# Optimization experiments

Hardware: AMD Instinct MI355X
Metric: run time of the kernel (lower is better)

Reference implementation:

```python
import jax, jax.numpy as jnp
import numpy as np

N, B, FD, D, MSG, SCN, H, FFN = 2048, 16, 128, 32, 32, 16, 4, 64
HD = D // H


def _lin(k, o, i, scale=0.05):
    kw, kb = jax.random.split(k)
    return (jax.random.normal(kw, (o, i), jnp.float32) * scale,
            jax.random.normal(kb, (o,), jnp.float32) * scale)


def setup_inputs() -> dict:
    key = jax.random.key(0)
    ks = jax.random.split(key, 24)
    inp = {}
    inp['src'] = jax.random.randint(ks[0], (B,), 0, N)
    inp['dst'] = jax.random.randint(ks[1], (B,), 0, N)
    inp['edge_feat'] = jax.random.normal(ks[2], (B, 3), jnp.float32)
    inp['timestamps'] = jax.random.uniform(ks[3], (B,), dtype=jnp.float32)
    inp['node_features'] = jax.random.normal(ks[4], (N, FD), jnp.float32)
    inp['adj'] = jnp.zeros((N, N), jnp.float32)  # unused: assume_identity_adj=True
    inp['memory'] = jax.random.normal(ks[5], (N, D), jnp.float32) * 0.1
    inp['W_emb'], inp['b_emb'] = _lin(ks[6], D, FD)
    inp['Wqkv'], inp['bqkv'] = _lin(ks[7], 3 * D, D)
    inp['Wo'], inp['bo'] = _lin(ks[8], D, D)
    inp['g1'] = jnp.ones((D,), jnp.float32); inp['be1'] = jnp.zeros((D,), jnp.float32)
    inp['g2'] = jnp.ones((D,), jnp.float32); inp['be2'] = jnp.zeros((D,), jnp.float32)
    inp['W_f1'], inp['b_f1'] = _lin(ks[9], FFN, D)
    inp['W_f2'], inp['b_f2'] = _lin(ks[10], D, FFN)
    inp['W_scn'], inp['b_scn'] = _lin(ks[11], SCN, D)
    inp['g_scn'] = jnp.ones((SCN,), jnp.float32); inp['be_scn'] = jnp.zeros((SCN,), jnp.float32)
    inp['W_e1'], inp['b_e1'] = _lin(ks[12], 32, 2 * SCN)
    inp['W_e2'], inp['b_e2'] = _lin(ks[13], 16, 32)
    inp['W_e3'], inp['b_e3'] = _lin(ks[14], 1, 16)
    inp['gru_Wih'], inp['gru_bih'] = _lin(ks[15], 3 * D, MSG)
    inp['gru_Whh'], inp['gru_bhh'] = _lin(ks[16], 3 * D, D)
    inp['W_m1'], inp['b_m1'] = _lin(ks[17], MSG, 2 * D + 3)
    inp['W_m2'], inp['b_m2'] = _lin(ks[18], MSG, MSG)
    return inp


def _ln(x, g, b):
    mu = x.mean(-1, keepdims=True)
    var = ((x - mu) ** 2).mean(-1, keepdims=True)
    return (x - mu) * jax.lax.rsqrt(var + 1e-5) * g + b


def _gru(x, h, Wih, Whh, bih, bhh):
    # torch.nn.GRUCell semantics
    gi = x @ Wih.T + bih
    gh = h @ Whh.T + bhh
    ir, iz, i_n = jnp.split(gi, 3, -1)
    hr, hz, h_n = jnp.split(gh, 3, -1)
    r = jax.nn.sigmoid(ir + hr)
    z = jax.nn.sigmoid(iz + hz)
    n = jnp.tanh(i_n + r * h_n)
    return (1.0 - z) * n + z * h


def _update_memory(memory, src, dst, edge_feat,
                   gru_Wih, gru_Whh, gru_bih, gru_bhh, W_m1, b_m1, W_m2, b_m2):
    # messages computed from pre-update memory (as in torch source)
    msg_in = jnp.concatenate([memory[src], memory[dst], edge_feat], axis=1)  # [B, 2D+3]
    messages = jax.nn.relu(msg_in @ W_m1.T + b_m1) @ W_m2.T + b_m2           # [B, MSG]

    def step(mem, inp):
        s, d, m = inp
        hs = _gru(m, mem[s], gru_Wih, gru_Whh, gru_bih, gru_bhh)
        mem = mem.at[s].set(hs)
        hd = _gru(m, mem[d], gru_Wih, gru_Whh, gru_bih, gru_bhh)  # sees updated mem if d==s earlier
        mem = mem.at[d].set(hd)
        return mem, None

    new_mem, _ = jax.lax.scan(step, memory, (src, dst, messages))
    return new_mem


def _edge_logits(node_features, src, dst,
                 W_emb, b_emb, Wqkv, bqkv, Wo, bo, g1, be1, g2, be2,
                 W_f1, b_f1, W_f2, b_f2, W_scn, b_scn, g_scn, be_scn,
                 W_e1, b_e1, W_e2, b_e2, W_e3, b_e3):
    x0 = node_features @ W_emb.T + b_emb                      # [N, D]
    x = jnp.broadcast_to(x0[None], (B, N, D))                 # [B, N, D]
    # --- Graph transformer layer (MHA, eval mode: dropout = identity) ---
    qkv = x @ Wqkv.T + bqkv                                   # [B, N, 3D]
    q, k, v = jnp.split(qkv, 3, -1)
    q = q.reshape(B, N, H, HD)
    k = k.reshape(B, N, H, HD)
    v = v.reshape(B, N, H, HD)
    scores = jnp.einsum('bqhd,bkhd->bhqk', q, k) / np.sqrt(HD)
    attn = jax.nn.softmax(scores, axis=-1)
    ao = jnp.einsum('bhqk,bkhd->bqhd', attn, v).reshape(B, N, D)
    ao = ao @ Wo.T + bo
    x = _ln(x + ao, g1, be1)
    ffn = jax.nn.gelu(x @ W_f1.T + b_f1, approximate=False) @ W_f2.T + b_f2
    x = _ln(x + ffn, g2, be2)
    # --- SCN layer (identity adjacency assumed) ---
    s_out = jax.nn.relu(_ln(x @ W_scn.T + b_scn, g_scn, be_scn))  # [B, N, SCN]
    bi = jnp.arange(B)
    src_emb = s_out[bi, src]
    dst_emb = s_out[bi, dst]
    h = jnp.concatenate([src_emb, dst_emb], axis=-1)
    h = jax.nn.relu(h @ W_e1.T + b_e1)
    h = jax.nn.relu(h @ W_e2.T + b_e2)
    return (h @ W_e3.T + b_e3).squeeze(-1)                    # [B]


def reference(src, dst, edge_feat, timestamps, node_features, adj, memory,
              W_emb, b_emb, Wqkv, bqkv, Wo, bo, g1, be1, g2, be2,
              W_f1, b_f1, W_f2, b_f2, W_scn, b_scn, g_scn, be_scn,
              W_e1, b_e1, W_e2, b_e2, W_e3, b_e3,
              gru_Wih, gru_bih, gru_Whh, gru_bhh, W_m1, b_m1, W_m2, b_m2):
    new_mem = _update_memory(memory, src, dst, edge_feat,
                             gru_Wih, gru_Whh, gru_bih, gru_bhh,
                             W_m1, b_m1, W_m2, b_m2)
    edge_logit = _edge_logits(node_features, src, dst,
                              W_emb, b_emb, Wqkv, bqkv, Wo, bo, g1, be1, g2, be2,
                              W_f1, b_f1, W_f2, b_f2, W_scn, b_scn, g_scn, be_scn,
                              W_e1, b_e1, W_e2, b_e2, W_e3, b_e3)
    return edge_logit, new_mem
```

## Files before the change

### kernel.cpp

```cpp
#include <hip/hip_runtime.h>
#include <math.h>

#define NN   2048
#define BB   16

#define WS_X0   0
#define WS_QT   65536
#define WS_KT   131072
#define WS_VT   196608
#define WS_PART 262144
#define WS_GI   268800

__device__ __forceinline__ float sigmoidf_(float x) { return 1.0f / (1.0f + __expf(-x)); }
__device__ __forceinline__ float tanhf_(float x) {
    float ex = __expf(2.0f * x);
    return 1.0f - 2.0f / (ex + 1.0f);
}
__device__ __forceinline__ float dot4_(float4 a, float4 b) {
    return a.x*b.x + a.y*b.y + a.z*b.z + a.w*b.w;
}

__global__ __launch_bounds__(256) void k1_embed_qkv_msg(
    const float* __restrict__ nf, const float* __restrict__ Wemb, const float* __restrict__ bemb,
    const float* __restrict__ Wqkv, const float* __restrict__ bqkv,
    const float* __restrict__ mem, const int* __restrict__ src, const int* __restrict__ dst,
    const float* __restrict__ ef,
    const float* __restrict__ Wm1, const float* __restrict__ bm1,
    const float* __restrict__ Wm2, const float* __restrict__ bm2,
    const float* __restrict__ Wih, const float* __restrict__ bih,
    float* __restrict__ ws, float* __restrict__ out)
{
    __shared__ float We_s[32 * 130];
    __shared__ float nf_s[8 * 130];
    __shared__ float x0_s[8 * 33];
    __shared__ float Wq_s[96 * 33];
    __shared__ __align__(16) float Wm1_s[2144];
    __shared__ float Wm2_s[32 * 33];
    __shared__ float Wih_s[96 * 33];
    __shared__ float min_s[67];
    __shared__ float mr_s[32];
    __shared__ float msg_s[32];

    const int t = threadIdx.x, bx = blockIdx.x;
    const bool domsg = (bx < 16);

    float4 rA[4], rB[3], rC;
    #pragma unroll
    for (int k = 0; k < 4; ++k) rA[k] = ((const float4*)Wemb)[t + 256 * k];
    #pragma unroll
    for (int k = 0; k < 3; ++k) rB[k] = ((const float4*)Wqkv)[t + 256 * k];
    rC = ((const float4*)nf)[bx * 256 + t];

    float4 rm1[3], rm2v, rih[3];
    float rminv = 0.f;
    if (domsg) {
        #pragma unroll
        for (int k = 0; k < 3; ++k) {
            int idx = t + 256 * k;
            rm1[k] = (idx < 536) ? ((const float4*)Wm1)[idx] : make_float4(0,0,0,0);
        }
        rm2v = ((const float4*)Wm2)[t];
        #pragma unroll
        for (int k = 0; k < 3; ++k) rih[k] = ((const float4*)Wih)[t + 256 * k];
        if (t < 67) {
            const int e = bx;
            rminv = (t < 32) ? mem[src[e] * 32 + t]
                  : (t < 64) ? mem[dst[e] * 32 + (t - 32)]
                             : ef[e * 3 + (t - 64)];
        }
    }

    if (bx >= 16 && bx < 80) {
        int g = (bx - 16) * 256 + t;
        ((float4*)(out + 16))[g] = ((const float4*)mem)[g];
    }

    #pragma unroll
    for (int k = 0; k < 4; ++k) {
        int idx = t + 256 * k;
        int r = idx >> 5, c = (idx & 31) * 4;
        We_s[r * 130 + c] = rA[k].x; We_s[r * 130 + c + 1] = rA[k].y;
        We_s[r * 130 + c + 2] = rA[k].z; We_s[r * 130 + c + 3] = rA[k].w;
    }
    #pragma unroll
    for (int k = 0; k < 3; ++k) {
        int idx = t + 256 * k;
        int r = idx >> 3, c = (idx & 7) * 4;
        Wq_s[r * 33 + c] = rB[k].x; Wq_s[r * 33 + c + 1] = rB[k].y;
        Wq_s[r * 33 + c + 2] = rB[k].z; Wq_s[r * 33 + c + 3] = rB[k].w;
    }
    {
        int r = t >> 5, c = (t & 31) * 4;
        nf_s[r * 130 + c] = rC.x; nf_s[r * 130 + c + 1] = rC.y;
        nf_s[r * 130 + c + 2] = rC.z; nf_s[r * 130 + c + 3] = rC.w;
    }
    if (domsg) {
        #pragma unroll
        for (int k = 0; k < 3; ++k) {
            int idx = t + 256 * k;
            if (idx < 536) ((float4*)Wm1_s)[idx] = rm1[k];
        }
        { int r = t >> 3, c = (t & 7) * 4;
          Wm2_s[r * 33 + c] = rm2v.x; Wm2_s[r * 33 + c + 1] = rm2v.y;
          Wm2_s[r * 33 + c + 2] = rm2v.z; Wm2_s[r * 33 + c + 3] = rm2v.w; }
        #pragma unroll
        for (int k = 0; k < 3; ++k) {
            int idx = t + 256 * k;
            int r = idx >> 3, c = (idx & 7) * 4;
            Wih_s[r * 33 + c] = rih[k].x; Wih_s[r * 33 + c + 1] = rih[k].y;
            Wih_s[r * 33 + c + 2] = rih[k].z; Wih_s[r * 33 + c + 3] = rih[k].w;
        }
        if (t < 67) min_s[t] = rminv;
    }
    __syncthreads();

    const int j = t >> 5, o = t & 31;
    const int n = bx * 8 + j;

    float acc = bemb[o];
    {
        const float2* Wr = (const float2*)&We_s[o * 130];
        const float2* Nr = (const float2*)&nf_s[j * 130];
        float sx = 0.f, sy = 0.f;
        #pragma unroll 16
        for (int i = 0; i < 64; ++i) {
            float2 w = Wr[i], x = Nr[i];
            sx += w.x * x.x; sy += w.y * x.y;
        }
        acc += sx + sy;
    }
    x0_s[j * 33 + o] = acc;
    ws[WS_X0 + n * 32 + o] = acc;
    if (domsg && t < 32) {
        float a1 = bm1[t];
        for (int i = 0; i < 67; ++i) a1 += Wm1_s[t * 67 + i] * min_s[i];
        mr_s[t] = fmaxf(a1, 0.f);
    }
    __syncthreads();

    #pragma unroll
    for (int c = 0; c < 3; ++c) {
        int oo = c * 32 + o;
        float a2 = bqkv[oo];
        #pragma unroll 8
        for (int i = 0; i < 32; ++i) a2 += Wq_s[oo * 33 + i] * x0_s[j * 33 + i];
        int h = o >> 3, d = o & 7;
        float* base = ws + (c == 0 ? WS_QT : (c == 1 ? WS_KT : WS_VT));
        base[h * 16384 + n * 8 + d] = a2;
    }
    if (domsg && t < 32) {
        float a2 = bm2[t];
        #pragma unroll 8
        for (int i = 0; i < 32; ++i) a2 += Wm2_s[t * 33 + i] * mr_s[i];
        msg_s[t] = a2;
    }
    __syncthreads();

    if (domsg && t < 96) {
        float a3 = bih[t];
        #pragma unroll 8
        for (int i = 0; i < 32; ++i) a3 += Wih_s[t * 33 + i] * msg_s[i];
        ws[WS_GI + bx * 96 + t] = a3;
    }
}

__global__ __launch_bounds__(256) void k2_attn(
    const int* __restrict__ src, const int* __restrict__ dst,
    float* __restrict__ ws)
{
    const int t = threadIdx.x, bx = blockIdx.x;
    const int s  = bx >> 2;
    const int ks = bx & 3;
    const int h  = t >> 6;
    const int l  = t & 63;

    const int e = s >> 1;
    const int n = (s & 1) ? dst[e] : src[e];

    const float* qg = ws + WS_QT + h * 16384 + n * 8;
    const float4 qa  = *(const float4*)qg;
    const float4 qb4 = *(const float4*)(qg + 4);
    const float* kbase = ws + WS_KT + h * 16384;
    const float* vbase = ws + WS_VT + h * 16384;

    float4 oa = make_float4(0.f, 0.f, 0.f, 0.f);
    float4 ob = make_float4(0.f, 0.f, 0.f, 0.f);
    float ssum = 0.f;
    const float scale = 0.35355339059327373f;

    #pragma unroll
    for (int i = 0; i < 8; ++i) {
        const int key = ks * 512 + i * 64 + l;
        const float4 ka = *(const float4*)(kbase + key * 8);
        const float4 kb = *(const float4*)(kbase + key * 8 + 4);
        const float sc = (dot4_(qa, ka) + dot4_(qb4, kb)) * scale;
        const float p = __expf(sc);
        ssum += p;
        const float4 va = *(const float4*)(vbase + key * 8);
        const float4 vb = *(const float4*)(vbase + key * 8 + 4);
        oa.x += p * va.x; oa.y += p * va.y; oa.z += p * va.z; oa.w += p * va.w;
        ob.x += p * vb.x; ob.y += p * vb.y; ob.z += p * vb.z; ob.w += p * vb.w;
    }

    #pragma unroll
    for (int m = 1; m <= 32; m <<= 1) {
        ssum += __shfl_xor(ssum, m);
        oa.x += __shfl_xor(oa.x, m); oa.y += __shfl_xor(oa.y, m);
        oa.z += __shfl_xor(oa.z, m); oa.w += __shfl_xor(oa.w, m);
        ob.x += __shfl_xor(ob.x, m); ob.y += __shfl_xor(ob.y, m);
        ob.z += __shfl_xor(ob.z, m); ob.w += __shfl_xor(ob.w, m);
    }
    if (l == 0) {
        float* p = ws + WS_PART + ((s * 4 + h) * 4 + ks) * 12;
        *(float4*)p       = oa;
        *(float4*)(p + 4) = ob;
        p[8] = ssum;
    }
}

__global__ __launch_bounds__(256, 1) void k34_post_scan(
    const int* __restrict__ src, const int* __restrict__ dst,
    const float* __restrict__ mem,
    const float* __restrict__ Wo, const float* __restrict__ bo,
    const float* __restrict__ g1, const float* __restrict__ be1,
    const float* __restrict__ Wf1, const float* __restrict__ bf1,
    const float* __restrict__ Wf2, const float* __restrict__ bf2,
    const float* __restrict__ g2, const float* __restrict__ be2,
    const float* __restrict__ Wscn, const float* __restrict__ bscn,
    const float* __restrict__ gscn, const float* __restrict__ bescn,
    const float* __restrict__ Whh, const float* __restrict__ bhh,
    const float* __restrict__ We1, const float* __restrict__ be1e,
    const float* __restrict__ We2, const float* __restrict__ be2e,
    const float* __restrict__ We3, const float* __restrict__ be3,
    float* __restrict__ ws, float* __restrict__ out)
{
    __shared__ float arow[32 * 33];
    __shared__ float x1s[32 * 33];
    __shared__ float fs[32 * 65];
    __shared__ __align__(16) float slots[32 * 36];
    __shared__ int nid_s[32], prev_s[32], round_s[32], last_s[32];
    __shared__ int list_s[32], cnt_s, maxr_s;

    const int t = threadIdx.x;
    const int j0 = t >> 5, o = t & 31;
    const int l = t & 63, w = t >> 6;
    const bool lowhalf = (l < 32);

    float4 w1[8], w2[8], w3[8];
    const int r2 = lowhalf ? l + 64 : l - 32;
    const int r3 = l + 32;
    #pragma unroll
    for (int c = 0; c < 8; ++c) {
        w1[c] = ((const float4*)Whh)[l * 8 + c];
        w2[c] = ((const float4*)Whh)[r2 * 8 + c];
        w3[c] = ((const float4*)Whh)[r3 * 8 + c];
    }
    const float b1 = bhh[l], b2 = bhh[r2], b3 = bhh[r3];

    if (t < 32) nid_s[t] = (t & 1) ? dst[t >> 1] : src[t >> 1];

    #pragma unroll 1
    for (int si = 0; si < 4; ++si) {
        const int jj = si * 8 + j0;
        const int ej = jj >> 1;
        const int n = (jj & 1) ? dst[ej] : src[ej];
        const int h = o >> 3, d = o & 7;
        float num = 0.f, den = 0.f;
        #pragma unroll
        for (int ks = 0; ks < 4; ++ks) {
            const float* p = ws + WS_PART + ((jj * 4 + h) * 4 + ks) * 12;
            num += p[d];
            den += p[8];
        }
        arow[jj * 33 + o] = num / den;
        fs[jj * 65 + o] = ws[WS_X0 + n * 32 + o];
    }
    __syncthreads();

    if (t < 32) {
        const int me = nid_s[t];
        int pv = -1, rd = 0;
        for (int j2 = 0; j2 < t; ++j2) if (nid_s[j2] == me) { pv = j2; ++rd; }
        prev_s[t] = pv; round_s[t] = rd;
        int isl = 1;
        for (int j2 = t + 1; j2 < 32; ++j2) if (nid_s[j2] == me) { isl = 0; break; }
        last_s[t] = isl;
        int mr = rd;
        #pragma unroll
        for (int m = 16; m >= 1; m >>= 1) mr = max(mr, __shfl_xor(mr, m, 32));
        if (t == 0) maxr_s = mr;
    }
    #pragma unroll
    for (int k = 0; k < 4; ++k) {
        int j2 = j0 + 8 * k;
        slots[j2 * 36 + o] = mem[nid_s[j2] * 32 + o];
    }

    {
        float4 wv[8];
        #pragma unroll
        for (int c = 0; c < 8; ++c) wv[c] = ((const float4*)(Wo + o * 32))[c];
        const float bv = bo[o], gv = g1[o], bev = be1[o];
        #pragma unroll 1
        for (int si = 0; si < 4; ++si) {
            const int jj = si * 8 + j0;
            float a = bv;
            #pragma unroll
            for (int c = 0; c < 8; ++c) {
                a = fmaf(wv[c].x, arow[jj * 33 + 4 * c],     a);
                a = fmaf(wv[c].y, arow[jj * 33 + 4 * c + 1], a);
                a = fmaf(wv[c].z, arow[jj * 33 + 4 * c + 2], a);
                a = fmaf(wv[c].w, arow[jj * 33 + 4 * c + 3], a);
            }
            float t1 = fs[jj * 65 + o] + a;
            float mu = t1;
            #pragma unroll
            for (int m = 16; m >= 1; m >>= 1) mu += __shfl_xor(mu, m, 32);
            mu *= (1.f / 32.f);
            float dv = t1 - mu;
            float var = dv * dv;
            #pragma unroll
            for (int m = 16; m >= 1; m >>= 1) var += __shfl_xor(var, m, 32);
            var *= (1.f / 32.f);
            x1s[jj * 33 + o] = dv * rsqrtf(var + 1e-5f) * gv + bev;
        }
    }
    __syncthreads();

    {
        float4 wa[8], wb[8];
        #pragma unroll
        for (int c = 0; c < 8; ++c) {
            wa[c] = ((const float4*)(Wf1 + o * 32))[c];
            wb[c] = ((const float4*)(Wf1 + (o + 32) * 32))[c];
        }
        const float ba = bf1[o], bb = bf1[o + 32];
        #pragma unroll 1
        for (int si = 0; si < 4; ++si) {
            const int jj = si * 8 + j0;
            float f0 = ba, f1 = bb;
            #pragma unroll
            for (int c = 0; c < 8; ++c) {
                const float xa = x1s[jj * 33 + 4 * c];
                const float xb = x1s[jj * 33 + 4 * c + 1];
                const float xc = x1s[jj * 33 + 4 * c + 2];
                const float xd = x1s[jj * 33 + 4 * c + 3];
                f0 = fmaf(wa[c].x, xa, f0); f0 = fmaf(wa[c].y, xb, f0);
                f0 = fmaf(wa[c].z, xc, f0); f0 = fmaf(wa[c].w, xd, f0);
                f1 = fmaf(wb[c].x, xa, f1); f1 = fmaf(wb[c].y, xb, f1);
                f1 = fmaf(wb[c].z, xc, f1); f1 = fmaf(wb[c].w, xd, f1);
            }
            fs[jj * 65 + o]      = 0.5f * f0 * (1.f + erff(f0 * 0.70710678118654752f));
            fs[jj * 65 + 32 + o] = 0.5f * f1 * (1.f + erff(f1 * 0.70710678118654752f));
        }
    }
    __syncthreads();

    {
        float4 wv[16];
        #pragma unroll
        for (int c = 0; c < 16; ++c) wv[c] = ((const float4*)(Wf2 + o * 64))[c];
        const float bv = bf2[o], gv = g2[o], bev = be2[o];
        #pragma unroll 1
        for (int si = 0; si < 4; ++si) {
            const int jj = si * 8 + j0;
            float f2 = bv;
            #pragma unroll
            for (int c = 0; c < 16; ++c) {
                f2 = fmaf(wv[c].x, fs[jj * 65 + 4 * c],     f2);
                f2 = fmaf(wv[c].y, fs[jj * 65 + 4 * c + 1], f2);
                f2 = fmaf(wv[c].z, fs[jj * 65 + 4 * c + 2], f2);
                f2 = fmaf(wv[c].w, fs[jj * 65 + 4 * c + 3], f2);
            }
            float t2 = x1s[jj * 33 + o] + f2;
            float mu2 = t2;
            #pragma unroll
            for (int m = 16; m >= 1; m >>= 1) mu2 += __shfl_xor(mu2, m, 32);
            mu2 *= (1.f / 32.f);
            float dv2 = t2 - mu2;
            float var2 = dv2 * dv2;
            #pragma unroll
            for (int m = 16; m >= 1; m >>= 1) var2 += __shfl_xor(var2, m, 32);
            var2 *= (1.f / 32.f);
            x1s[jj * 33 + o] = dv2 * rsqrtf(var2 + 1e-5f) * gv + bev;
        }
    }
    __syncthreads();

    if (o < 16) {
        float4 wv[8];
        #pragma unroll
        for (int c = 0; c < 8; ++c) wv[c] = ((const float4*)(Wscn + o * 32))[c];
        const float bv = bscn[o], gv = gscn[o], bev = bescn[o];
        #pragma unroll 1
        for (int si = 0; si < 4; ++si) {
            const int jj = si * 8 + j0;
            float sc = bv;
            #pragma unroll
            for (int c = 0; c < 8; ++c) {
                sc = fmaf(wv[c].x, x1s[jj * 33 + 4 * c],     sc);
                sc = fmaf(wv[c].y, x1s[jj * 33 + 4 * c + 1], sc);
                sc = fmaf(wv[c].z, x1s[jj * 33 + 4 * c + 2], sc);
                sc = fmaf(wv[c].w, x1s[jj * 33 + 4 * c + 3], sc);
            }
            float m16 = sc;
            #pragma unroll
            for (int m = 8; m >= 1; m >>= 1) m16 += __shfl_xor(m16, m, 16);
            m16 *= (1.f / 16.f);
            float d16 = sc - m16;
            float v16 = d16 * d16;
            #pragma unroll
            for (int m = 8; m >= 1; m >>= 1) v16 += __shfl_xor(v16, m, 16);
            v16 *= (1.f / 16.f);
            float sv = d16 * rsqrtf(v16 + 1e-5f) * gv + bev;
            arow[(jj >> 1) * 33 + (jj & 1) * 16 + o] = fmaxf(sv, 0.f);
        }
    }
    __syncthreads();

    {
        float4 wv[8];
        #pragma unroll
        for (int c = 0; c < 8; ++c) wv[c] = ((const float4*)(We1 + o * 32))[c];
        const float bv = be1e[o];
        #pragma unroll 1
        for (int k = 0; k < 2; ++k) {
            int e = j0 + 8 * k;
            float acc = bv;
            #pragma unroll
            for (int c = 0; c < 8; ++c) {
                acc = fmaf(wv[c].x, arow[e * 33 + 4 * c],     acc);
                acc = fmaf(wv[c].y, arow[e * 33 + 4 * c + 1], acc);
                acc = fmaf(wv[c].z, arow[e * 33 + 4 * c + 2], acc);
                acc = fmaf(wv[c].w, arow[e * 33 + 4 * c + 3], acc);
            }
            fs[e * 33 + o] = fmaxf(acc, 0.f);
        }
    }
    __syncthreads();

    {
        const int e = t >> 4, o2 = t & 15;
        float4 wv[8];
        #pragma unroll
        for (int c = 0; c < 8; ++c) wv[c] = ((const float4*)(We2 + o2 * 32))[c];
        float acc = be2e[o2];
        #pragma unroll
        for (int c = 0; c < 8; ++c) {
            acc = fmaf(wv[c].x, fs[e * 33 + 4 * c],     acc);
            acc = fmaf(wv[c].y, fs[e * 33 + 4 * c + 1], acc);
            acc = fmaf(wv[c].z, fs[e * 33 + 4 * c + 2], acc);
            acc = fmaf(wv[c].w, fs[e * 33 + 4 * c + 3], acc);
        }
        __syncthreads();
        fs[600 + e * 17 + o2] = fmaxf(acc, 0.f);
    }
    __syncthreads();

    if (t < 16) {
        float4 w3a = ((const float4*)We3)[0], w3b = ((const float4*)We3)[1];
        float4 w3c = ((const float4*)We3)[2], w3d = ((const float4*)We3)[3];
        float acc = be3[0];
        acc = fmaf(w3a.x, fs[600 + t * 17 + 0], acc);  acc = fmaf(w3a.y, fs[600 + t * 17 + 1], acc);
        acc = fmaf(w3a.z, fs[600 + t * 17 + 2], acc);  acc = fmaf(w3a.w, fs[600 + t * 17 + 3], acc);
        acc = fmaf(w3b.x, fs[600 + t * 17 + 4], acc);  acc = fmaf(w3b.y, fs[600 + t * 17 + 5], acc);
        acc = fmaf(w3b.z, fs[600 + t * 17 + 6], acc);  acc = fmaf(w3b.w, fs[600 + t * 17 + 7], acc);
        acc = fmaf(w3c.x, fs[600 + t * 17 + 8], acc);  acc = fmaf(w3c.y, fs[600 + t * 17 + 9], acc);
        acc = fmaf(w3c.z, fs[600 + t * 17 + 10], acc); acc = fmaf(w3c.w, fs[600 + t * 17 + 11], acc);
        acc = fmaf(w3d.x, fs[600 + t * 17 + 12], acc); acc = fmaf(w3d.y, fs[600 + t * 17 + 13], acc);
        acc = fmaf(w3d.z, fs[600 + t * 17 + 14], acc); acc = fmaf(w3d.w, fs[600 + t * 17 + 15], acc);
        out[t] = acc;
    }

    const int maxr = maxr_s;
    for (int r = 0; r <= maxr; ++r) {
        if (t < 64) {
            bool act = (t < 32) && (round_s[t] == r);
            unsigned long long mask = __ballot(act);
            if (act) {
                int pos = __popcll(mask & ((1ull << t) - 1ull));
                list_s[pos] = t;
            }
            if (t == 0) cnt_s = (int)__popcll(mask);
        }
        __syncthreads();
        const int cnt = cnt_s;
        #pragma unroll 1
        for (int pi = w; 2 * pi < cnt; pi += 4) {
            const int sA = list_s[2 * pi];
            const bool doB = (2 * pi + 1 < cnt);
            const int sB = doB ? list_s[2 * pi + 1] : sA;
            const int inA = (prev_s[sA] < 0) ? sA : prev_s[sA];
            const int inB = (prev_s[sB] < 0) ? sB : prev_s[sB];
            const int sX = lowhalf ? sA : sB;
            const int eX = sX >> 1;
            const float ir  = ws[WS_GI + eX * 96 + o];
            const float iz  = ws[WS_GI + eX * 96 + 32 + o];
            const float inn = ws[WS_GI + eX * 96 + 64 + o];
            float acc1 = b1, acc2 = b2, acc3 = b3;
            #pragma unroll
            for (int c = 0; c < 8; ++c) {
                const float4 hs4 = *(const float4*)&slots[inA * 36 + 4 * c];
                const float4 hd4 = *(const float4*)&slots[inB * 36 + 4 * c];
                acc1 += dot4_(w1[c], hs4);
                const float4 hm = lowhalf ? hs4 : hd4;
                acc2 += dot4_(w2[c], hm);
                acc3 += dot4_(w3[c], hd4);
            }
            const float shv = __shfl_xor(lowhalf ? acc3 : acc1, 32);
            const float hr = lowhalf ? acc1 : acc2;
            const float hz = shv;
            const float hn = lowhalf ? acc2 : acc3;
            const float rr = sigmoidf_(ir + hr);
            const float z = sigmoidf_(iz + hz);
            const float nn = tanhf_(inn + rr * hn);
            const float hold = slots[(lowhalf ? inA : inB) * 36 + o];
            const float hnew = (1.f - z) * nn + z * hold;
            if (lowhalf || doB) slots[sX * 36 + o] = hnew;
        }
        __syncthreads();
    }

    #pragma unroll
    for (int k = 0; k < 4; ++k) {
        int j2 = j0 + 8 * k;
        if (last_s[j2]) out[16 + nid_s[j2] * 32 + o] = slots[j2 * 36 + o];
    }
}

extern "C" void kernel_launch(void* const* d_in, const int* in_sizes, int n_in,
                              void* d_out, int out_size, void* d_ws, size_t ws_size,
                              hipStream_t stream)
{
    (void)in_sizes; (void)n_in; (void)out_size; (void)ws_size;
    const int*   src   = (const int*)d_in[0];
    const int*   dst   = (const int*)d_in[1];
    const float* ef    = (const float*)d_in[2];
    const float* nf    = (const float*)d_in[4];
    const float* mem   = (const float*)d_in[6];
    const float* Wemb  = (const float*)d_in[7];
    const float* bemb  = (const float*)d_in[8];
    const float* Wqkv  = (const float*)d_in[9];
    const float* bqkv  = (const float*)d_in[10];
    const float* Wo    = (const float*)d_in[11];
    const float* bo    = (const float*)d_in[12];
    const float* g1    = (const float*)d_in[13];
    const float* be1   = (const float*)d_in[14];
    const float* g2    = (const float*)d_in[15];
    const float* be2   = (const float*)d_in[16];
    const float* Wf1   = (const float*)d_in[17];
    const float* bf1   = (const float*)d_in[18];
    const float* Wf2   = (const float*)d_in[19];
    const float* bf2   = (const float*)d_in[20];
    const float* Wscn  = (const float*)d_in[21];
    const float* bscn  = (const float*)d_in[22];
    const float* gscn  = (const float*)d_in[23];
    const float* bescn = (const float*)d_in[24];
    const float* We1   = (const float*)d_in[25];
    const float* be1e  = (const float*)d_in[26];
    const float* We2   = (const float*)d_in[27];
    const float* be2e  = (const float*)d_in[28];
    const float* We3   = (const float*)d_in[29];
    const float* be3   = (const float*)d_in[30];
    const float* Wih   = (const float*)d_in[31];
    const float* bih   = (const float*)d_in[32];
    const float* Whh   = (const float*)d_in[33];
    const float* bhh   = (const float*)d_in[34];
    const float* Wm1   = (const float*)d_in[35];
    const float* bm1   = (const float*)d_in[36];
    const float* Wm2   = (const float*)d_in[37];
    const float* bm2   = (const float*)d_in[38];
    float* out = (float*)d_out;
    float* ws  = (float*)d_ws;

    hipLaunchKernelGGL(k1_embed_qkv_msg, dim3(256), dim3(256), 0, stream,
        nf, Wemb, bemb, Wqkv, bqkv, mem, src, dst, ef, Wm1, bm1, Wm2, bm2, Wih, bih, ws, out);
    hipLaunchKernelGGL(k2_attn, dim3(128), dim3(256), 0, stream, src, dst, ws);
    hipLaunchKernelGGL(k34_post_scan, dim3(1), dim3(256), 0, stream,
        src, dst, mem, Wo, bo, g1, be1, Wf1, bf1, Wf2, bf2, g2, be2,
        Wscn, bscn, gscn, bescn, Whh, bhh, We1, be1e, We2, be2e, We3, be3, ws, out);
}
```

Baseline: 178.0 us.

## Fuse attention with per-row post-processing and drop key-split partials

Attention now runs in one block per query row (32 blocks, not 128 key-split blocks). The same block then performs the output projection, both layernorms, the FFN and the SCN projection, writing SCN outputs to the workspace. The single-block final kernel keeps only the edge MLP and the GRU scan, so the serial post-processing moves into parallel blocks. In exchange, attention parallelism drops fourfold, and each block walks all 2048 keys serially.

Result: no change. 177.1 us (-0.5%).

```diff
diff --git a/kernel.cpp b/kernel.cpp
--- a/kernel.cpp
+++ b/kernel.cpp
@@ -8,8 +8,8 @@
 #define WS_QT   65536
 #define WS_KT   131072
 #define WS_VT   196608
-#define WS_PART 262144
 #define WS_GI   268800
+#define WS_SOUT 270336
 
 __device__ __forceinline__ float sigmoidf_(float x) { return 1.0f / (1.0f + __expf(-x)); }
 __device__ __forceinline__ float tanhf_(float x) {
@@ -164,18 +164,49 @@
     }
 }
 
-__global__ __launch_bounds__(256) void k2_attn(
+__global__ __launch_bounds__(256, 1) void k2_attn_post(
     const int* __restrict__ src, const int* __restrict__ dst,
+    const float* __restrict__ Wo, const float* __restrict__ bo,
+    const float* __restrict__ g1, const float* __restrict__ be1,
+    const float* __restrict__ Wf1, const float* __restrict__ bf1,
+    const float* __restrict__ Wf2, const float* __restrict__ bf2,
+    const float* __restrict__ g2, const float* __restrict__ be2,
+    const float* __restrict__ Wscn, const float* __restrict__ bscn,
+    const float* __restrict__ gscn, const float* __restrict__ bescn,
     float* __restrict__ ws)
 {
-    const int t = threadIdx.x, bx = blockIdx.x;
-    const int s  = bx >> 2;
-    const int ks = bx & 3;
-    const int h  = t >> 6;
-    const int l  = t & 63;
-
+    __shared__ float arow_s[32];
+    __shared__ float x1_s[32];
+    __shared__ float fs_s[64];
+    __shared__ float x2_s[32];
+
+    const int t = threadIdx.x, s = blockIdx.x;
+    const int h = t >> 6, l = t & 63;
     const int e = s >> 1;
     const int n = (s & 1) ? dst[e] : src[e];
+
+    float4 wo_r[8], wf2_r[16], wf1_r[8], wscn_r[8];
+    float x0v = 0.f, bo_v = 0.f, g1_v = 0.f, be1_v = 0.f, bf2_v = 0.f;
+    float g2_v = 0.f, be2_v = 0.f, bf1_v = 0.f, bscn_v = 0.f, gscn_v = 0.f, bescn_v = 0.f;
+    if (t < 32) {
+        #pragma unroll
+        for (int c = 0; c < 8; ++c)  wo_r[c]  = ((const float4*)(Wo  + t * 32))[c];
+        #pragma unroll
+        for (int c = 0; c < 16; ++c) wf2_r[c] = ((const float4*)(Wf2 + t * 64))[c];
+        x0v = ws[WS_X0 + n * 32 + t];
+        bo_v = bo[t]; g1_v = g1[t]; be1_v = be1[t];
+        bf2_v = bf2[t]; g2_v = g2[t]; be2_v = be2[t];
+    }
+    if (t < 64) {
+        #pragma unroll
+        for (int c = 0; c < 8; ++c) wf1_r[c] = ((const float4*)(Wf1 + t * 32))[c];
+        bf1_v = bf1[t];
+    }
+    if (t < 16) {
+        #pragma unroll
+        for (int c = 0; c < 8; ++c) wscn_r[c] = ((const float4*)(Wscn + t * 32))[c];
+        bscn_v = bscn[t]; gscn_v = gscn[t]; bescn_v = bescn[t];
+    }
 
     const float* qg = ws + WS_QT + h * 16384 + n * 8;
     const float4 qa  = *(const float4*)qg;
@@ -188,9 +219,9 @@
     float ssum = 0.f;
     const float scale = 0.35355339059327373f;
 
-    #pragma unroll
-    for (int i = 0; i < 8; ++i) {
-        const int key = ks * 512 + i * 64 + l;
+    #pragma unroll 4
+    for (int i = 0; i < 32; ++i) {
+        const int key = i * 64 + l;
         const float4 ka = *(const float4*)(kbase + key * 8);
         const float4 kb = *(const float4*)(kbase + key * 8 + 4);
         const float sc = (dot4_(qa, ka) + dot4_(qb4, kb)) * scale;
@@ -201,7 +232,6 @@
         oa.x += p * va.x; oa.y += p * va.y; oa.z += p * va.z; oa.w += p * va.w;
         ob.x += p * vb.x; ob.y += p * vb.y; ob.z += p * vb.z; ob.w += p * vb.w;
     }
-
     #pragma unroll
     for (int m = 1; m <= 32; m <<= 1) {
         ssum += __shfl_xor(ssum, m);
@@ -211,32 +241,105 @@
         ob.z += __shfl_xor(ob.z, m); ob.w += __shfl_xor(ob.w, m);
     }
     if (l == 0) {
-        float* p = ws + WS_PART + ((s * 4 + h) * 4 + ks) * 12;
-        *(float4*)p       = oa;
-        *(float4*)(p + 4) = ob;
-        p[8] = ssum;
+        const float inv = 1.0f / ssum;
+        float* ap = arow_s + h * 8;
+        ap[0] = oa.x * inv; ap[1] = oa.y * inv; ap[2] = oa.z * inv; ap[3] = oa.w * inv;
+        ap[4] = ob.x * inv; ap[5] = ob.y * inv; ap[6] = ob.z * inv; ap[7] = ob.w * inv;
+    }
+    __syncthreads();
+
+    if (t < 64) {
+        float x1 = 0.f;
+        if (t < 32) {
+            float a = bo_v;
+            #pragma unroll
+            for (int c = 0; c < 8; ++c) {
+                a = fmaf(wo_r[c].x, arow_s[4 * c],     a);
+                a = fmaf(wo_r[c].y, arow_s[4 * c + 1], a);
+                a = fmaf(wo_r[c].z, arow_s[4 * c + 2], a);
+                a = fmaf(wo_r[c].w, arow_s[4 * c + 3], a);
+            }
+            const float t1 = x0v + a;
+            float mu = t1;
+            #pragma unroll
+            for (int m = 16; m >= 1; m >>= 1) mu += __shfl_xor(mu, m, 32);
+            mu *= (1.f / 32.f);
+            const float dv = t1 - mu;
+            float var = dv * dv;
+            #pragma unroll
+            for (int m = 16; m >= 1; m >>= 1) var += __shfl_xor(var, m, 32);
+            var *= (1.f / 32.f);
+            x1 = dv * rsqrtf(var + 1e-5f) * g1_v + be1_v;
+            x1_s[t] = x1;
+        }
+        {
+            float f = bf1_v;
+            #pragma unroll
+            for (int c = 0; c < 8; ++c) {
+                f = fmaf(wf1_r[c].x, x1_s[4 * c],     f);
+                f = fmaf(wf1_r[c].y, x1_s[4 * c + 1], f);
+                f = fmaf(wf1_r[c].z, x1_s[4 * c + 2], f);
+                f = fmaf(wf1_r[c].w, x1_s[4 * c + 3], f);
+            }
+            fs_s[t] = 0.5f * f * (1.f + erff(f * 0.70710678118654752f));
+        }
+        if (t < 32) {
+            float f2 = bf2_v;
+            #pragma unroll
+            for (int c = 0; c < 16; ++c) {
+                f2 = fmaf(wf2_r[c].x, fs_s[4 * c],     f2);
+                f2 = fmaf(wf2_r[c].y, fs_s[4 * c + 1], f2);
+                f2 = fmaf(wf2_r[c].z, fs_s[4 * c + 2], f2);
+                f2 = fmaf(wf2_r[c].w, fs_s[4 * c + 3], f2);
+            }
+            const float t2 = x1 + f2;
+            float mu2 = t2;
+            #pragma unroll
+            for (int m = 16; m >= 1; m >>= 1) mu2 += __shfl_xor(mu2, m, 32);
+            mu2 *= (1.f / 32.f);
+            const float dv2 = t2 - mu2;
+            float var2 = dv2 * dv2;
+            #pragma unroll
+            for (int m = 16; m >= 1; m >>= 1) var2 += __shfl_xor(var2, m, 32);
+            var2 *= (1.f / 32.f);
+            x2_s[t] = dv2 * rsqrtf(var2 + 1e-5f) * g2_v + be2_v;
+        }
+        if (t < 16) {
+            float sc = bscn_v;
+            #pragma unroll
+            for (int c = 0; c < 8; ++c) {
+                sc = fmaf(wscn_r[c].x, x2_s[4 * c],     sc);
+                sc = fmaf(wscn_r[c].y, x2_s[4 * c + 1], sc);
+                sc = fmaf(wscn_r[c].z, x2_s[4 * c + 2], sc);
+                sc = fmaf(wscn_r[c].w, x2_s[4 * c + 3], sc);
+            }
+            float m16 = sc;
+            #pragma unroll
+            for (int m = 8; m >= 1; m >>= 1) m16 += __shfl_xor(m16, m, 16);
+            m16 *= (1.f / 16.f);
+            const float d16 = sc - m16;
+            float v16 = d16 * d16;
+            #pragma unroll
+            for (int m = 8; m >= 1; m >>= 1) v16 += __shfl_xor(v16, m, 16);
+            v16 *= (1.f / 16.f);
+            const float sv = d16 * rsqrtf(v16 + 1e-5f) * gscn_v + bescn_v;
+            ws[WS_SOUT + s * 16 + t] = fmaxf(sv, 0.f);
+        }
     }
 }
 
-__global__ __launch_bounds__(256, 1) void k34_post_scan(
+__global__ __launch_bounds__(256, 1) void k3_edge_scan(
     const int* __restrict__ src, const int* __restrict__ dst,
     const float* __restrict__ mem,
-    const float* __restrict__ Wo, const float* __restrict__ bo,
-    const float* __restrict__ g1, const float* __restrict__ be1,
-    const float* __restrict__ Wf1, const float* __restrict__ bf1,
-    const float* __restrict__ Wf2, const float* __restrict__ bf2,
-    const float* __restrict__ g2, const float* __restrict__ be2,
-    const float* __restrict__ Wscn, const float* __restrict__ bscn,
-    const float* __restrict__ gscn, const float* __restrict__ bescn,
     const float* __restrict__ Whh, const float* __restrict__ bhh,
     const float* __restrict__ We1, const float* __restrict__ be1e,
     const float* __restrict__ We2, const float* __restrict__ be2e,
     const float* __restrict__ We3, const float* __restrict__ be3,
     float* __restrict__ ws, float* __restrict__ out)
 {
-    __shared__ float arow[32 * 33];
-    __shared__ float x1s[32 * 33];
-    __shared__ float fs[32 * 65];
+    __shared__ float cat_s[16 * 33];
+    __shared__ float h1_s[16 * 33];
+    __shared__ float h2_s[16 * 17];
     __shared__ __align__(16) float slots[32 * 36];
     __shared__ int nid_s[32], prev_s[32], round_s[32], last_s[32];
     __shared__ int list_s[32], cnt_s, maxr_s;
@@ -257,23 +360,22 @@
     }
     const float b1 = bhh[l], b2 = bhh[r2], b3 = bhh[r3];
 
+    float4 we1_r[8], we2_r[8];
+    #pragma unroll
+    for (int c = 0; c < 8; ++c) {
+        we1_r[c] = ((const float4*)(We1 + o * 32))[c];
+        we2_r[c] = ((const float4*)(We2 + (t & 15) * 32))[c];
+    }
+    const float be1e_v = be1e[o];
+
     if (t < 32) nid_s[t] = (t & 1) ? dst[t >> 1] : src[t >> 1];
 
-    #pragma unroll 1
-    for (int si = 0; si < 4; ++si) {
-        const int jj = si * 8 + j0;
-        const int ej = jj >> 1;
-        const int n = (jj & 1) ? dst[ej] : src[ej];
-        const int h = o >> 3, d = o & 7;
-        float num = 0.f, den = 0.f;
-        #pragma unroll
-        for (int ks = 0; ks < 4; ++ks) {
-            const float* p = ws + WS_PART + ((jj * 4 + h) * 4 + ks) * 12;
-            num += p[d];
-            den += p[8];
-        }
-        arow[jj * 33 + o] = num / den;
-        fs[jj * 65 + o] = ws[WS_X0 + n * 32 + o];
+    #pragma unroll
+    for (int k = 0; k < 2; ++k) {
+        const int idx = t + 256 * k;
+        const int e = idx >> 5, i = idx & 31;
+        cat_s[e * 33 + i] = (i < 16) ? ws[WS_SOUT + (2 * e) * 16 + i]
+                                     : ws[WS_SOUT + (2 * e + 1) * 16 + (i - 16)];
     }
     __syncthreads();
 
@@ -292,193 +394,52 @@
     }
     #pragma unroll
     for (int k = 0; k < 4; ++k) {
-        int j2 = j0 + 8 * k;
+        const int j2 = j0 + 8 * k;
         slots[j2 * 36 + o] = mem[nid_s[j2] * 32 + o];
     }
-
-    {
-        float4 wv[8];
-        #pragma unroll
-        for (int c = 0; c < 8; ++c) wv[c] = ((const float4*)(Wo + o * 32))[c];
-        const float bv = bo[o], gv = g1[o], bev = be1[o];
-        #pragma unroll 1
-        for (int si = 0; si < 4; ++si) {
-            const int jj = si * 8 + j0;
-            float a = bv;
-            #pragma unroll
-            for (int c = 0; c < 8; ++c) {
-                a = fmaf(wv[c].x, arow[jj * 33 + 4 * c],     a);
-                a = fmaf(wv[c].y, arow[jj * 33 + 4 * c + 1], a);
-                a = fmaf(wv[c].z, arow[jj * 33 + 4 * c + 2], a);
-                a = fmaf(wv[c].w, arow[jj * 33 + 4 * c + 3], a);
-            }
-            float t1 = fs[jj * 65 + o] + a;
-            float mu = t1;
-            #pragma unroll
-            for (int m = 16; m >= 1; m >>= 1) mu += __shfl_xor(mu, m, 32);
-            mu *= (1.f / 32.f);
-            float dv = t1 - mu;
-            float var = dv * dv;
-            #pragma unroll
-            for (int m = 16; m >= 1; m >>= 1) var += __shfl_xor(var, m, 32);
-            var *= (1.f / 32.f);
-            x1s[jj * 33 + o] = dv * rsqrtf(var + 1e-5f) * gv + bev;
-        }
-    }
-    __syncthreads();
-
-    {
-        float4 wa[8], wb[8];
+    #pragma unroll 1
+    for (int k = 0; k < 2; ++k) {
+        const int e = j0 + 8 * k;
+        float acc = be1e_v;
         #pragma unroll
         for (int c = 0; c < 8; ++c) {
-            wa[c] = ((const float4*)(Wf1 + o * 32))[c];
-            wb[c] = ((const float4*)(Wf1 + (o + 32) * 32))[c];
-        }
-        const float ba = bf1[o], bb = bf1[o + 32];
-        #pragma unroll 1
-        for (int si = 0; si < 4; ++si) {
-            const int jj = si * 8 + j0;
-            float f0 = ba, f1 = bb;
-            #pragma unroll
-            for (int c = 0; c < 8; ++c) {
-                const float xa = x1s[jj * 33 + 4 * c];
-                const float xb = x1s[jj * 33 + 4 * c + 1];
-                const float xc = x1s[jj * 33 + 4 * c + 2];
-                const float xd = x1s[jj * 33 + 4 * c + 3];
-                f0 = fmaf(wa[c].x, xa, f0); f0 = fmaf(wa[c].y, xb, f0);
-                f0 = fmaf(wa[c].z, xc, f0); f0 = fmaf(wa[c].w, xd, f0);
-                f1 = fmaf(wb[c].x, xa, f1); f1 = fmaf(wb[c].y, xb, f1);
-                f1 = fmaf(wb[c].z, xc, f1); f1 = fmaf(wb[c].w, xd, f1);
-            }
-            fs[jj * 65 + o]      = 0.5f * f0 * (1.f + erff(f0 * 0.70710678118654752f));
-            fs[jj * 65 + 32 + o] = 0.5f * f1 * (1.f + erff(f1 * 0.70710678118654752f));
-        }
-    }
-    __syncthreads();
-
-    {
-        float4 wv[16];
-        #pragma unroll
-        for (int c = 0; c < 16; ++c) wv[c] = ((const float4*)(Wf2 + o * 64))[c];
-        const float bv = bf2[o], gv = g2[o], bev = be2[o];
-        #pragma unroll 1
-        for (int si = 0; si < 4; ++si) {
-            const int jj = si * 8 + j0;
-            float f2 = bv;
-            #pragma unroll
-            for (int c = 0; c < 16; ++c) {
-                f2 = fmaf(wv[c].x, fs[jj * 65 + 4 * c],     f2);
-                f2 = fmaf(wv[c].y, fs[jj * 65 + 4 * c + 1], f2);
-                f2 = fmaf(wv[c].z, fs[jj * 65 + 4 * c + 2], f2);
-                f2 = fmaf(wv[c].w, fs[jj * 65 + 4 * c + 3], f2);
-            }
-            float t2 = x1s[jj * 33 + o] + f2;
-            float mu2 = t2;
-            #pragma unroll
-            for (int m = 16; m >= 1; m >>= 1) mu2 += __shfl_xor(mu2, m, 32);
-            mu2 *= (1.f / 32.f);
-            float dv2 = t2 - mu2;
-            float var2 = dv2 * dv2;
-            #pragma unroll
-            for (int m = 16; m >= 1; m >>= 1) var2 += __shfl_xor(var2, m, 32);
-            var2 *= (1.f / 32.f);
-            x1s[jj * 33 + o] = dv2 * rsqrtf(var2 + 1e-5f) * gv + bev;
-        }
-    }
-    __syncthreads();
-
-    if (o < 16) {
-        float4 wv[8];
-        #pragma unroll
-        for (int c = 0; c < 8; ++c) wv[c] = ((const float4*)(Wscn + o * 32))[c];
-        const float bv = bscn[o], gv = gscn[o], bev = bescn[o];
-        #pragma unroll 1
-        for (int si = 0; si < 4; ++si) {
-            const int jj = si * 8 + j0;
-            float sc = bv;
-            #pragma unroll
-            for (int c = 0; c < 8; ++c) {
-                sc = fmaf(wv[c].x, x1s[jj * 33 + 4 * c],     sc);
-                sc = fmaf(wv[c].y, x1s[jj * 33 + 4 * c + 1], sc);
-                sc = fmaf(wv[c].z, x1s[jj * 33 + 4 * c + 2], sc);
-                sc = fmaf(wv[c].w, x1s[jj * 33 + 4 * c + 3], sc);
-            }
-            float m16 = sc;
-            #pragma unroll
-            for (int m = 8; m >= 1; m >>= 1) m16 += __shfl_xor(m16, m, 16);
-            m16 *= (1.f / 16.f);
-            float d16 = sc - m16;
-            float v16 = d16 * d16;
-            #pragma unroll
-            for (int m = 8; m >= 1; m >>= 1) v16 += __shfl_xor(v16, m, 16);
-            v16 *= (1.f / 16.f);
-            float sv = d16 * rsqrtf(v16 + 1e-5f) * gv + bev;
-            arow[(jj >> 1) * 33 + (jj & 1) * 16 + o] = fmaxf(sv, 0.f);
-        }
-    }
-    __syncthreads();
-
-    {
-        float4 wv[8];
-        #pragma unroll
-        for (int c = 0; c < 8; ++c) wv[c] = ((const float4*)(We1 + o * 32))[c];
-        const float bv = be1e[o];
-        #pragma unroll 1
-        for (int k = 0; k < 2; ++k) {
-            int e = j0 + 8 * k;
-            float acc = bv;
-            #pragma unroll
-            for (int c = 0; c < 8; ++c) {
-                acc = fmaf(wv[c].x, arow[e * 33 + 4 * c],     acc);
-                acc = fmaf(wv[c].y, arow[e * 33 + 4 * c + 1], acc);
-                acc = fmaf(wv[c].z, arow[e * 33 + 4 * c + 2], acc);
-                acc = fmaf(wv[c].w, arow[e * 33 + 4 * c + 3], acc);
-            }
-            fs[e * 33 + o] = fmaxf(acc, 0.f);
-        }
+            acc = fmaf(we1_r[c].x, cat_s[e * 33 + 4 * c],     acc);
+            acc = fmaf(we1_r[c].y, cat_s[e * 33 + 4 * c + 1], acc);
+            acc = fmaf(we1_r[c].z, cat_s[e * 33 + 4 * c + 2], acc);
+            acc = fmaf(we1_r[c].w, cat_s[e * 33 + 4 * c + 3], acc);
+        }
+        h1_s[e * 33 + o] = fmaxf(acc, 0.f);
     }
     __syncthreads();
 
     {
         const int e = t >> 4, o2 = t & 15;
-        float4 wv[8];
-        #pragma unroll
-        for (int c = 0; c < 8; ++c) wv[c] = ((const float4*)(We2 + o2 * 32))[c];
         float acc = be2e[o2];
         #pragma unroll
         for (int c = 0; c < 8; ++c) {
-            acc = fmaf(wv[c].x, fs[e * 33 + 4 * c],     acc);
-            acc = fmaf(wv[c].y, fs[e * 33 + 4 * c + 1], acc);
-            acc = fmaf(wv[c].z, fs[e * 33 + 4 * c + 2], acc);
-            acc = fmaf(wv[c].w, fs[e * 33 + 4 * c + 3], acc);
-        }
-        __syncthreads();
-        fs[600 + e * 17 + o2] = fmaxf(acc, 0.f);
+            acc = fmaf(we2_r[c].x, h1_s[e * 33 + 4 * c],     acc);
+            acc = fmaf(we2_r[c].y, h1_s[e * 33 + 4 * c + 1], acc);
+            acc = fmaf(we2_r[c].z, h1_s[e * 33 + 4 * c + 2], acc);
+            acc = fmaf(we2_r[c].w, h1_s[e * 33 + 4 * c + 3], acc);
+        }
+        h2_s[e * 17 + o2] = fmaxf(acc, 0.f);
     }
     __syncthreads();
 
     if (t < 16) {
-        float4 w3a = ((const float4*)We3)[0], w3b = ((const float4*)We3)[1];
-        float4 w3c = ((const float4*)We3)[2], w3d = ((const float4*)We3)[3];
         float acc = be3[0];
-        acc = fmaf(w3a.x, fs[600 + t * 17 + 0], acc);  acc = fmaf(w3a.y, fs[600 + t * 17 + 1], acc);
-        acc = fmaf(w3a.z, fs[600 + t * 17 + 2], acc);  acc = fmaf(w3a.w, fs[600 + t * 17 + 3], acc);
-        acc = fmaf(w3b.x, fs[600 + t * 17 + 4], acc);  acc = fmaf(w3b.y, fs[600 + t * 17 + 5], acc);
-        acc = fmaf(w3b.z, fs[600 + t * 17 + 6], acc);  acc = fmaf(w3b.w, fs[600 + t * 17 + 7], acc);
-        acc = fmaf(w3c.x, fs[600 + t * 17 + 8], acc);  acc = fmaf(w3c.y, fs[600 + t * 17 + 9], acc);
-        acc = fmaf(w3c.z, fs[600 + t * 17 + 10], acc); acc = fmaf(w3c.w, fs[600 + t * 17 + 11], acc);
-        acc = fmaf(w3d.x, fs[600 + t * 17 + 12], acc); acc = fmaf(w3d.y, fs[600 + t * 17 + 13], acc);
-        acc = fmaf(w3d.z, fs[600 + t * 17 + 14], acc); acc = fmaf(w3d.w, fs[600 + t * 17 + 15], acc);
+        #pragma unroll
+        for (int i = 0; i < 16; ++i) acc = fmaf(We3[i], h2_s[t * 17 + i], acc);
         out[t] = acc;
     }
 
     const int maxr = maxr_s;
     for (int r = 0; r <= maxr; ++r) {
         if (t < 64) {
-            bool act = (t < 32) && (round_s[t] == r);
-            unsigned long long mask = __ballot(act);
+            const bool act = (t < 32) && (round_s[t] == r);
+            const unsigned long long mask = __ballot(act);
             if (act) {
-                int pos = __popcll(mask & ((1ull << t) - 1ull));
+                const int pos = __popcll(mask & ((1ull << t) - 1ull));
                 list_s[pos] = t;
             }
             if (t == 0) cnt_s = (int)__popcll(mask);
@@ -523,7 +484,7 @@
 
     #pragma unroll
     for (int k = 0; k < 4; ++k) {
-        int j2 = j0 + 8 * k;
+        const int j2 = j0 + 8 * k;
         if (last_s[j2]) out[16 + nid_s[j2] * 32 + o] = slots[j2 * 36 + o];
     }
 }
@@ -575,8 +536,9 @@
 
     hipLaunchKernelGGL(k1_embed_qkv_msg, dim3(256), dim3(256), 0, stream,
         nf, Wemb, bemb, Wqkv, bqkv, mem, src, dst, ef, Wm1, bm1, Wm2, bm2, Wih, bih, ws, out);
-    hipLaunchKernelGGL(k2_attn, dim3(128), dim3(256), 0, stream, src, dst, ws);
-    hipLaunchKernelGGL(k34_post_scan, dim3(1), dim3(256), 0, stream,
-        src, dst, mem, Wo, bo, g1, be1, Wf1, bf1, Wf2, bf2, g2, be2,
-        Wscn, bscn, gscn, bescn, Whh, bhh, We1, be1e, We2, be2e, We3, be3, ws, out);
+    hipLaunchKernelGGL(k2_attn_post, dim3(32), dim3(256), 0, stream,
+        src, dst, Wo, bo, g1, be1, Wf1, bf1, Wf2, bf2, g2, be2,
+        Wscn, bscn, gscn, bescn, ws);
+    hipLaunchKernelGGL(k3_edge_scan, dim3(1), dim3(256), 0, stream,
+        src, dst, mem, Whh, bhh, We1, be1e, We2, be2e, We3, be3, ws, out);
 }
```
